# Optimization experiments

Hardware: AMD Instinct MI355X
Metric: run time of the kernel (lower is better)

## Reference

```python
import jax, jax.numpy as jnp
import numpy as np
import math

B, T, D = 2, 2048, 2048
N_HEADS, N_KV, HEAD_DIM = 16, 4, 128
INTER = 8192
MAX_POS = 4096
ROPE_BASE = 10000.0
EPS = 1e-6


def _rope_tables():
    inv_freq = 1.0 / (ROPE_BASE ** (jnp.arange(0, HEAD_DIM, 2, dtype=jnp.float32) / HEAD_DIM))
    t = jnp.arange(MAX_POS, dtype=jnp.float32)
    freqs = jnp.einsum('i,j->ij', t, inv_freq)          # [MAX_POS, HEAD_DIM//2]
    emb = jnp.concatenate([freqs, freqs], axis=-1)      # [MAX_POS, HEAD_DIM]
    return jnp.cos(emb), jnp.sin(emb)


def _apply_rope(x, cos, sin):
    # x: [B,H,T,Dh]; cos/sin: [B,T,Dh] (gathered by position_ids)
    c = cos[:, None, :, :]
    s = sin[:, None, :, :]
    x1 = x[..., ::2]
    x2 = x[..., 1::2]
    x_rot = jnp.stack([-x2, x1], axis=-1).reshape(x.shape)  # interleave(-x2, x1)
    return x * c + x_rot * s


def _rms_norm(x, w):
    var = jnp.mean(x * x, axis=-1, keepdims=True)
    return w * (x * jax.lax.rsqrt(var + EPS))


def setup_inputs() -> dict:
    key = jax.random.key(0)
    ks = jax.random.split(key, 10)
    s = 0.02
    hidden_states = jax.random.normal(ks[0], (B, T, D), dtype=jnp.float32)
    # additive causal mask
    causal = jnp.tril(jnp.ones((T, T), dtype=bool))
    attention_mask = jnp.where(causal, 0.0, -1e9).astype(jnp.float32)[None, None]
    position_ids = jnp.arange(B * T).reshape(B, T)  # values < MAX_POS
    return {
        'hidden_states': hidden_states,
        'attention_mask': attention_mask,
        'position_ids': position_ids,
        'attn_norm_w': jnp.ones((D,), jnp.float32),
        'mlp_norm_w': jnp.ones((D,), jnp.float32),
        'wq': jax.random.normal(ks[1], (D, N_HEADS * HEAD_DIM), jnp.float32) * s,
        'wk': jax.random.normal(ks[2], (D, N_KV * HEAD_DIM), jnp.float32) * s,
        'wv': jax.random.normal(ks[3], (D, N_KV * HEAD_DIM), jnp.float32) * s,
        'wo': jax.random.normal(ks[4], (N_HEADS * HEAD_DIM, D), jnp.float32) * s,
        'gate_w': jax.random.normal(ks[5], (D, D), jnp.float32) * s,
        'gate_b': jnp.zeros((D,), jnp.float32),
        'fc1_w': jax.random.normal(ks[6], (D, INTER), jnp.float32) * s,
        'fc2_w': jax.random.normal(ks[7], (INTER, D), jnp.float32) * s,
    }


def reference(hidden_states, attention_mask, position_ids, attn_norm_w, mlp_norm_w,
              wq, wk, wv, wo, gate_w, gate_b, fc1_w, fc2_w):
    b, t, _ = hidden_states.shape
    residual = hidden_states
    h = _rms_norm(hidden_states, attn_norm_w)

    # elementwise sigmoid output gate: [B,T,D] -> [B,H,T,Dh]
    gate = jax.nn.sigmoid(h @ gate_w + gate_b)
    gate = gate.reshape(b, t, N_HEADS, HEAD_DIM).transpose(0, 2, 1, 3)

    q = (h @ wq).reshape(b, t, N_HEADS, HEAD_DIM).transpose(0, 2, 1, 3)
    k = (h @ wk).reshape(b, t, N_KV, HEAD_DIM).transpose(0, 2, 1, 3)
    v = (h @ wv).reshape(b, t, N_KV, HEAD_DIM).transpose(0, 2, 1, 3)

    cos_t, sin_t = _rope_tables()
    cos = cos_t[position_ids]  # [B,T,Dh]
    sin = sin_t[position_ids]
    q = _apply_rope(q, cos, sin)
    k = _apply_rope(k, cos, sin)

    n_rep = N_HEADS // N_KV
    k = jnp.repeat(k, n_rep, axis=1)  # GQA expand to [B,H,T,Dh]
    v = jnp.repeat(v, n_rep, axis=1)

    scores = jnp.einsum('bhqd,bhkd->bhqk', q, k) / math.sqrt(HEAD_DIM)
    scores = scores + attention_mask
    attn = jax.nn.softmax(scores, axis=-1)
    out = jnp.einsum('bhqk,bhkd->bhqd', attn, v) * gate
    out = out.transpose(0, 2, 1, 3).reshape(b, t, N_HEADS * HEAD_DIM) @ wo

    h = residual + out
    residual = h
    h2 = _rms_norm(h, mlp_norm_w)
    mlp_out = jax.nn.silu(h2 @ fc1_w) @ fc2_w
    return residual + mlp_out
```

## Files before the change

### kernel.cpp

```cpp
#include <hip/hip_runtime.h>
#include <hip/hip_bf16.h>
#include <cstdint>
#include <cstddef>

#define BB 2
#define TT 2048
#define DD 2048
#define NH 16
#define NKV 4
#define HD 128
#define NI 8192
#define MM (BB*TT)

typedef __bf16 bf16x8 __attribute__((ext_vector_type(8)));
typedef float  f32x4  __attribute__((ext_vector_type(4)));

__device__ __forceinline__ void gload_lds16(const void* g, void* l) {
  __builtin_amdgcn_global_load_lds((__attribute__((address_space(1))) void*)g,
                                   (__attribute__((address_space(3))) void*)l,
                                   16, 0, 0);
}

__device__ __forceinline__ int xcd_swizzle(int wg, int nwg) {
  int xcd = wg & 7;
  int l = wg >> 3;
  int q = nwg >> 3, r = nwg & 7;
  return (xcd < r ? xcd * (q + 1) : r * (q + 1) + (xcd - r) * q) + l;
}

__global__ __launch_bounds__(128) void rope_tables_k(float* __restrict__ cosT,
                                                     float* __restrict__ sinT) {
  int pos = blockIdx.x;
  int d = threadIdx.x;
  int f = d & 63;
  float inv = powf(10000.0f, -((float)(2 * f)) / 128.0f);
  float ang = inv * (float)pos;
  cosT[pos * 128 + d] = cosf(ang);
  sinT[pos * 128 + d] = sinf(ang);
}

template <typename TIN>
__global__ __launch_bounds__(256) void transpose_to_bf16_k(const TIN* __restrict__ in,
                                                           __bf16* __restrict__ out,
                                                           int R, int C) {
  __shared__ float t[32][33];
  int c0 = blockIdx.x * 32, r0 = blockIdx.y * 32;
  int tx = threadIdx.x & 31;
  int ty = threadIdx.x >> 5;
#pragma unroll
  for (int i = 0; i < 4; i++) {
    int r = ty + i * 8;
    t[r][tx] = (float)in[(size_t)(r0 + r) * C + c0 + tx];
  }
  __syncthreads();
#pragma unroll
  for (int i = 0; i < 4; i++) {
    int r = ty + i * 8;
    out[(size_t)(c0 + r) * R + r0 + tx] = (__bf16)t[tx][r];
  }
}

__global__ __launch_bounds__(256) void rmsnorm_k(const float* __restrict__ x,
                                                 const float* __restrict__ w,
                                                 __bf16* __restrict__ out) {
  int row = blockIdx.x;
  const float* xr = x + (size_t)row * DD;
  int t = threadIdx.x;
  float4 a = ((const float4*)xr)[2 * t];
  float4 b = ((const float4*)xr)[2 * t + 1];
  float ss = a.x * a.x + a.y * a.y + a.z * a.z + a.w * a.w +
             b.x * b.x + b.y * b.y + b.z * b.z + b.w * b.w;
#pragma unroll
  for (int off = 32; off; off >>= 1) ss += __shfl_xor(ss, off, 64);
  __shared__ float red[4];
  if ((t & 63) == 0) red[t >> 6] = ss;
  __syncthreads();
  float tot = red[0] + red[1] + red[2] + red[3];
  float rs = rsqrtf(tot * (1.0f / DD) + 1e-6f);
  const float4 w1 = ((const float4*)w)[2 * t];
  const float4 w2 = ((const float4*)w)[2 * t + 1];
  bf16x8 ov;
  ov[0] = (__bf16)(a.x * rs * w1.x);
  ov[1] = (__bf16)(a.y * rs * w1.y);
  ov[2] = (__bf16)(a.z * rs * w1.z);
  ov[3] = (__bf16)(a.w * rs * w1.w);
  ov[4] = (__bf16)(b.x * rs * w2.x);
  ov[5] = (__bf16)(b.y * rs * w2.y);
  ov[6] = (__bf16)(b.z * rs * w2.z);
  ov[7] = (__bf16)(b.w * rs * w2.w);
  *(bf16x8*)(out + (size_t)row * DD + t * 8) = ov;
}

enum { G_QG = 0, G_RES = 1, G_SILU = 2, G_PART = 3 };

template <int EPI>
__global__ __launch_bounds__(512) void gemm256_k(
    const __bf16* __restrict__ A, const __bf16* __restrict__ Bt,
    __bf16* __restrict__ outB, float* __restrict__ outF,
    __bf16* __restrict__ outQ, __bf16* __restrict__ outG,
    const float* __restrict__ bias, const float* __restrict__ residual,
    const float* __restrict__ cosT, const float* __restrict__ sinT,
    const int* __restrict__ posids, int N, int K, int ldk, float oscale) {
  __shared__ __align__(16) __bf16 Ab[3][256 * 32];
  __shared__ __align__(16) __bf16 Bb[3][256 * 32];
  const int tid = threadIdx.x;
  const int lane = tid & 63;
  const int wid = tid >> 6;
  const int wr = wid >> 2;
  const int wc = wid & 3;
  const int fr = lane & 15;
  const int fg = lane >> 4;

  const int nwg = gridDim.x * gridDim.y;
  int wg = xcd_swizzle(blockIdx.y * gridDim.x + blockIdx.x, nwg);
  const int bx = wg % gridDim.x, by = wg / gridDim.x;
  const int m0 = by * 256;
  const int n0 = bx * 256;
  const int kz = blockIdx.z;
  const int kBase = kz * K;

  const int srow0 = wid * 32 + (lane >> 2);
  const int scol = (((lane & 3) ^ ((lane >> 3) & 3)) << 3);
  const __bf16* aS0 = A + (size_t)(m0 + srow0) * ldk + kBase + scol;
  const __bf16* aS1 = aS0 + (size_t)16 * ldk;
  const __bf16* bS0 = Bt + (size_t)(n0 + srow0) * ldk + kBase + scol;
  const __bf16* bS1 = bS0 + (size_t)16 * ldk;
  const int e0 = (wid * 2) * 512;
  const int e1 = (wid * 2 + 1) * 512;

  const int nt = K / 32;

#define STG_A0(kt, s) gload_lds16(aS0 + (kt) * 32, &Ab[(s)][e0]);
#define STG_A1(kt, s) gload_lds16(aS1 + (kt) * 32, &Ab[(s)][e1]);
#define STG_B0(kt, s) gload_lds16(bS0 + (kt) * 32, &Bb[(s)][e0]);
#define STG_B1(kt, s) gload_lds16(bS1 + (kt) * 32, &Bb[(s)][e1]);

  STG_A0(0, 0); STG_A1(0, 0); STG_B0(0, 0); STG_B1(0, 0);
  STG_A0(1, 1); STG_A1(1, 1); STG_B0(1, 1); STG_B1(1, 1);
  asm volatile("s_waitcnt vmcnt(4)" ::: "memory");
  __builtin_amdgcn_s_barrier();

  f32x4 acc[8][4];
#pragma unroll
  for (int i = 0; i < 8; i++)
#pragma unroll
    for (int j = 0; j < 4; j++) acc[i][j] = (f32x4){0.f, 0.f, 0.f, 0.f};

  const int asl = (fg ^ ((fr >> 1) & 3)) * 8;

  for (int t = 0; t < nt; ++t) {
    const int s = t % 3;
    const int sn = (t + 2) % 3;
    const bool dostage = (t + 2 < nt);
    bf16x8 bfr[4];

    {
      bf16x8 af[2];
#pragma unroll
      for (int mi = 0; mi < 2; mi++)
        af[mi] = *(const bf16x8*)&Ab[s][(wr * 128 + mi * 16 + fr) * 32 + asl];
#pragma unroll
      for (int ni = 0; ni < 4; ni++)
        bfr[ni] = *(const bf16x8*)&Bb[s][(wc * 64 + ni * 16 + fr) * 32 + asl];
      if (dostage) STG_A0(t + 2, sn);
      __builtin_amdgcn_s_barrier();
      asm volatile("s_waitcnt lgkmcnt(0)" ::: "memory");
      __builtin_amdgcn_sched_barrier(0);
      __builtin_amdgcn_s_setprio(1);
#pragma unroll
      for (int mi = 0; mi < 2; mi++)
#pragma unroll
        for (int ni = 0; ni < 4; ni++)
          acc[mi][ni] =
              __builtin_amdgcn_mfma_f32_16x16x32_bf16(af[mi], bfr[ni], acc[mi][ni], 0, 0, 0);
      __builtin_amdgcn_s_setprio(0);
      __builtin_amdgcn_s_barrier();
    }
#pragma unroll
    for (int ph = 1; ph < 4; ph++) {
      bf16x8 af[2];
#pragma unroll
      for (int mi = 0; mi < 2; mi++)
        af[mi] = *(const bf16x8*)&Ab[s][(wr * 128 + (ph * 2 + mi) * 16 + fr) * 32 + asl];
      if (dostage) {
        if (ph == 1) { STG_A1(t + 2, sn); }
        else if (ph == 2) { STG_B0(t + 2, sn); }
        else { STG_B1(t + 2, sn); }
      }
      __builtin_amdgcn_s_barrier();
      asm volatile("s_waitcnt lgkmcnt(0)" ::: "memory");
      __builtin_amdgcn_sched_barrier(0);
      __builtin_amdgcn_s_setprio(1);
#pragma unroll
      for (int mi = 0; mi < 2; mi++)
#pragma unroll
        for (int ni = 0; ni < 4; ni++)
          acc[ph * 2 + mi][ni] = __builtin_amdgcn_mfma_f32_16x16x32_bf16(
              af[mi], bfr[ni], acc[ph * 2 + mi][ni], 0, 0, 0);
      __builtin_amdgcn_s_setprio(0);
      if (ph == 3) {
        if (dostage) {
          asm volatile("s_waitcnt vmcnt(4)" ::: "memory");
        } else {
          asm volatile("s_waitcnt vmcnt(0)" ::: "memory");
        }
      }
      __builtin_amdgcn_s_barrier();
    }
  }
#undef STG_A0
#undef STG_A1
#undef STG_B0
#undef STG_B1

#pragma unroll
  for (int mi = 0; mi < 8; mi++) {
    const int row = m0 + wr * 128 + mi * 16 + fg * 4;
#pragma unroll
    for (int ni = 0; ni < 4; ni++) {
      const int col = n0 + wc * 64 + ni * 16 + fr;
#pragma unroll
      for (int j = 0; j < 4; j++) {
        float v = acc[mi][ni][j];
        const int r = row + j;
        if constexpr (EPI == G_QG) {
          float vp = __shfl_xor(v, 1, 64);
          if (n0 < 2048) {
            int pos = posids[r];
            int d = col & 127;
            float c = cosT[pos * 128 + d], sn2 = sinT[pos * 128 + d];
            float o = (col & 1) ? (v * c + vp * sn2) : (v * c - vp * sn2);
            outQ[(size_t)r * 2048 + col] = (__bf16)(o * oscale);
          } else {
            float xx = v + bias[col - 2048];
            outG[(size_t)r * 2048 + (col - 2048)] = (__bf16)(1.0f / (1.0f + expf(-xx)));
          }
        } else if constexpr (EPI == G_RES) {
          outF[(size_t)r * N + col] = v + residual[(size_t)r * N + col];
        } else if constexpr (EPI == G_SILU) {
          outB[(size_t)r * N + col] = (__bf16)(v / (1.0f + expf(-v)));
        } else {
          outB[(size_t)(kz * MM + r) * N + col] = (__bf16)v;
        }
      }
    }
  }
}

__global__ __launch_bounds__(256) void combine_k(const __bf16* __restrict__ parts,
                                                 const float* __restrict__ res,
                                                 float* __restrict__ out) {
  size_t i = ((size_t)blockIdx.x * 256 + threadIdx.x) * 8;
  bf16x8 p0 = *(const bf16x8*)&parts[i];
  bf16x8 p1 = *(const bf16x8*)&parts[(size_t)MM * 2048 + i];
  float4 a = *(const float4*)&res[i];
  float4 b = *(const float4*)&res[i + 4];
  float4 o0, o1;
  o0.x = (float)p0[0] + (float)p1[0] + a.x;
  o0.y = (float)p0[1] + (float)p1[1] + a.y;
  o0.z = (float)p0[2] + (float)p1[2] + a.z;
  o0.w = (float)p0[3] + (float)p1[3] + a.w;
  o1.x = (float)p0[4] + (float)p1[4] + b.x;
  o1.y = (float)p0[5] + (float)p1[5] + b.y;
  o1.z = (float)p0[6] + (float)p1[6] + b.z;
  o1.w = (float)p0[7] + (float)p1[7] + b.w;
  *(float4*)&out[i] = o0;
  *(float4*)&out[i + 4] = o1;
}

__global__ __launch_bounds__(256) void combine_rms_k(const __bf16* __restrict__ parts,
                                                     const float* __restrict__ res,
                                                     const float* __restrict__ w,
                                                     float* __restrict__ h1,
                                                     __bf16* __restrict__ h2) {
  const int row = blockIdx.x;
  const int t = threadIdx.x;
  const size_t i = (size_t)row * 2048 + t * 8;
  bf16x8 p0 = *(const bf16x8*)&parts[i];
  bf16x8 p1 = *(const bf16x8*)&parts[(size_t)MM * 2048 + i];
  float4 a = *(const float4*)&res[i];
  float4 b = *(const float4*)&res[i + 4];
  float v[8];
  v[0] = (float)p0[0] + (float)p1[0] + a.x;
  v[1] = (float)p0[1] + (float)p1[1] + a.y;
  v[2] = (float)p0[2] + (float)p1[2] + a.z;
  v[3] = (float)p0[3] + (float)p1[3] + a.w;
  v[4] = (float)p0[4] + (float)p1[4] + b.x;
  v[5] = (float)p0[5] + (float)p1[5] + b.y;
  v[6] = (float)p0[6] + (float)p1[6] + b.z;
  v[7] = (float)p0[7] + (float)p1[7] + b.w;
  float4 o0 = {v[0], v[1], v[2], v[3]};
  float4 o1 = {v[4], v[5], v[6], v[7]};
  *(float4*)&h1[i] = o0;
  *(float4*)&h1[i + 4] = o1;
  float ss = 0.f;
#pragma unroll
  for (int k = 0; k < 8; k++) ss += v[k] * v[k];
#pragma unroll
  for (int off = 32; off; off >>= 1) ss += __shfl_xor(ss, off, 64);
  __shared__ float red[4];
  if ((t & 63) == 0) red[t >> 6] = ss;
  __syncthreads();
  float tot = red[0] + red[1] + red[2] + red[3];
  float rs = rsqrtf(tot * (1.0f / DD) + 1e-6f);
  const float4 w1 = ((const float4*)w)[2 * t];
  const float4 w2 = ((const float4*)w)[2 * t + 1];
  bf16x8 ov;
  ov[0] = (__bf16)(v[0] * rs * w1.x);
  ov[1] = (__bf16)(v[1] * rs * w1.y);
  ov[2] = (__bf16)(v[2] * rs * w1.z);
  ov[3] = (__bf16)(v[3] * rs * w1.w);
  ov[4] = (__bf16)(v[4] * rs * w2.x);
  ov[5] = (__bf16)(v[5] * rs * w2.y);
  ov[6] = (__bf16)(v[6] * rs * w2.z);
  ov[7] = (__bf16)(v[7] * rs * w2.w);
  *(bf16x8*)(h2 + i) = ov;
}

__global__ __launch_bounds__(256) void gemm_kv_k(
    const __bf16* __restrict__ A, const __bf16* __restrict__ Bt,
    __bf16* __restrict__ kOut, __bf16* __restrict__ vOut,
    const float* __restrict__ cosT, const float* __restrict__ sinT,
    const int* __restrict__ posids, int K) {
  __shared__ __align__(16) __bf16 As[128 * 32];
  __shared__ __align__(16) __bf16 Bs[128 * 32];
  const int tid = threadIdx.x;
  const int lane = tid & 63;
  const int w = tid >> 6;
  const int wm = w >> 1, wn = w & 1;

  const int nwg = gridDim.x * gridDim.y;
  int wg = xcd_swizzle(blockIdx.y * gridDim.x + blockIdx.x, nwg);
  const int bx = wg % gridDim.x, by = wg / gridDim.x;
  const int m0 = by * 128;
  const int n0 = bx * 128;

  const int lr = lane >> 2;
  const int lc = (lane & 3) * 8;
  const __bf16* aSrc = A + (size_t)(m0 + 32 * w + lr) * K + lc;
  const __bf16* bSrc = Bt + (size_t)(n0 + 32 * w + lr) * K + lc;
  __bf16* aDst = &As[w * 1024];
  __bf16* bDst = &Bs[w * 1024];

  f32x4 acc[4][4];
#pragma unroll
  for (int i = 0; i < 4; i++)
#pragma unroll
    for (int j = 0; j < 4; j++) acc[i][j] = (f32x4){0.f, 0.f, 0.f, 0.f};

  const int fr = lane & 15;
  const int fc = (lane >> 4) * 8;

  for (int k0 = 0; k0 < K; k0 += 32) {
    __syncthreads();
    gload_lds16(aSrc + k0, aDst);
    gload_lds16(aSrc + k0 + (size_t)16 * K, aDst + 512);
    gload_lds16(bSrc + k0, bDst);
    gload_lds16(bSrc + k0 + (size_t)16 * K, bDst + 512);
    asm volatile("s_waitcnt vmcnt(0)" ::: "memory");
    __syncthreads();

    bf16x8 af[4], bfg[4];
#pragma unroll
    for (int i = 0; i < 4; i++)
      af[i] = *(const bf16x8*)&As[(wm * 64 + i * 16 + fr) * 32 + fc];
#pragma unroll
    for (int i = 0; i < 4; i++)
      bfg[i] = *(const bf16x8*)&Bs[(wn * 64 + i * 16 + fr) * 32 + fc];
#pragma unroll
    for (int mi = 0; mi < 4; mi++)
#pragma unroll
      for (int ni = 0; ni < 4; ni++)
        acc[mi][ni] =
            __builtin_amdgcn_mfma_f32_16x16x32_bf16(af[mi], bfg[ni], acc[mi][ni], 0, 0, 0);
  }

  const int fg = lane >> 4;
#pragma unroll
  for (int mi = 0; mi < 4; mi++) {
#pragma unroll
    for (int ni = 0; ni < 4; ni++) {
#pragma unroll
      for (int j = 0; j < 4; j++) {
        int row = m0 + wm * 64 + mi * 16 + fg * 4 + j;
        int col = n0 + wn * 64 + ni * 16 + fr;
        float v = acc[mi][ni][j];
        float vp = __shfl_xor(v, 1, 64);
        if (col < 512) {
          int pos = posids[row];
          int d = col & 127;
          float c = cosT[pos * 128 + d];
          float s = sinT[pos * 128 + d];
          float o = (col & 1) ? (v * c + vp * s) : (v * c - vp * s);
          kOut[(size_t)row * 512 + col] = (__bf16)o;
        } else {
          vOut[(size_t)row * 512 + (col - 512)] = (__bf16)v;
        }
      }
    }
  }
}

__global__ __launch_bounds__(256) void attn_k(const __bf16* __restrict__ Q,
                                              const __bf16* __restrict__ Kb,
                                              const __bf16* __restrict__ Vt,
                                              const __bf16* __restrict__ Gate,
                                              __bf16* __restrict__ Out) {
  __shared__ __align__(16) __bf16 Ks[2][64 * 128];
  __shared__ __align__(16) __bf16 Vs[2][128 * 64];
  __shared__ __align__(16) __bf16 Ps[4][16 * 64];
  const int tid = threadIdx.x;
  const int lane = tid & 63;
  const int w = tid >> 6;
  const int fr = lane & 15;
  const int fg = lane >> 4;

  const int nwg = gridDim.x * gridDim.y;
  int wg = xcd_swizzle(blockIdx.y * gridDim.x + blockIdx.x, nwg);
  const int qb = wg % gridDim.x;
  const int bh = wg / gridDim.x;
  const int q0 = qb * 64;
  const int b = bh >> 4, h = bh & 15;
  const int g = h >> 2;

  const size_t qrow = (size_t)(b * TT + q0 + w * 16 + fr);
  bf16x8 qf[4];
#pragma unroll
  for (int kt = 0; kt < 4; kt++)
    qf[kt] = *(const bf16x8*)&Q[qrow * 2048 + h * 128 + kt * 32 + fg * 8];

  const __bf16* kPtr[4];
  const __bf16* vPtr[4];
#pragma unroll
  for (int i = 0; i < 4; i++) {
    int krow = w * 16 + i * 4 + (lane >> 4);
    int kcol8 = (lane & 15) ^ (krow & 15);
    kPtr[i] = Kb + (size_t)(b * TT + krow) * 512 + g * 128 + kcol8 * 8;
    int dloc = w * 32 + i * 8 + (lane >> 3);
    int kv8 = (lane & 7) ^ (dloc & 7);
    vPtr[i] = Vt + (size_t)(g * 128 + dloc) * (size_t)MM + b * TT + kv8 * 8;
  }

  f32x4 o[8];
#pragma unroll
  for (int i = 0; i < 8; i++) o[i] = (f32x4){0.f, 0.f, 0.f, 0.f};
  float mrow[4] = {-3e38f, -3e38f, -3e38f, -3e38f};
  float lrow[4] = {0.f, 0.f, 0.f, 0.f};

  const int nsteps = qb + 1;

#pragma unroll
  for (int i = 0; i < 4; i++) {
    gload_lds16(kPtr[i], &Ks[0][w * 2048 + i * 512]);
    gload_lds16(vPtr[i], &Vs[0][w * 2048 + i * 512]);
  }
  __syncthreads();

  for (int t = 0; t < nsteps; t++) {
    const int cur = t & 1;
    const int kb = t * 64;
    if (t + 1 < nsteps) {
      const int nb = kb + 64;
#pragma unroll
      for (int i = 0; i < 4; i++) {
        gload_lds16(kPtr[i] + (size_t)nb * 512, &Ks[cur ^ 1][w * 2048 + i * 512]);
        gload_lds16(vPtr[i] + nb, &Vs[cur ^ 1][w * 2048 + i * 512]);
      }
    }

    f32x4 s[4];
#pragma unroll
    for (int nc = 0; nc < 4; nc++) s[nc] = (f32x4){0.f, 0.f, 0.f, 0.f};
#pragma unroll
    for (int nc = 0; nc < 4; nc++)
#pragma unroll
      for (int kt = 0; kt < 4; kt++) {
        bf16x8 kf = *(const bf16x8*)&Ks[cur][(nc * 16 + fr) * 128 + (((kt * 4 + fg) ^ fr) << 3)];
        s[nc] = __builtin_amdgcn_mfma_f32_16x16x32_bf16(qf[kt], kf, s[nc], 0, 0, 0);
      }

    float alpha[4];
#pragma unroll
    for (int j = 0; j < 4; j++) {
      const int qr = q0 + w * 16 + fg * 4 + j;
      float pv[4];
#pragma unroll
      for (int nc = 0; nc < 4; nc++) {
        int kc = kb + nc * 16 + fr;
        float val = s[nc][j];
        if (kc > qr) val = -1e9f;
        pv[nc] = val;
      }
      float tmx = fmaxf(fmaxf(pv[0], pv[1]), fmaxf(pv[2], pv[3]));
      tmx = fmaxf(tmx, __shfl_xor(tmx, 1, 64));
      tmx = fmaxf(tmx, __shfl_xor(tmx, 2, 64));
      tmx = fmaxf(tmx, __shfl_xor(tmx, 4, 64));
      tmx = fmaxf(tmx, __shfl_xor(tmx, 8, 64));
      float mnew = fmaxf(mrow[j], tmx);
      alpha[j] = __expf(mrow[j] - mnew);
      mrow[j] = mnew;
      float rsum = 0.f;
      const int q = fg * 4 + j;
#pragma unroll
      for (int nc = 0; nc < 4; nc++) {
        float e = __expf(pv[nc] - mnew);
        rsum += e;
        Ps[w][q * 64 + (((nc * 2 + (fr >> 3)) ^ (q & 7)) << 3) + (fr & 7)] = (__bf16)e;
      }
      rsum += __shfl_xor(rsum, 1, 64);
      rsum += __shfl_xor(rsum, 2, 64);
      rsum += __shfl_xor(rsum, 4, 64);
      rsum += __shfl_xor(rsum, 8, 64);
      lrow[j] = lrow[j] * alpha[j] + rsum;
    }
#pragma unroll
    for (int nd = 0; nd < 8; nd++)
#pragma unroll
      for (int j = 0; j < 4; j++) o[nd][j] *= alpha[j];

    bf16x8 pa[2];
#pragma unroll
    for (int sl = 0; sl < 2; sl++)
      pa[sl] = *(const bf16x8*)&Ps[w][fr * 64 + (((sl * 4 + fg) ^ (fr & 7)) << 3)];
#pragma unroll
    for (int nd = 0; nd < 8; nd++)
#pragma unroll
      for (int sl = 0; sl < 2; sl++) {
        bf16x8 vf =
            *(const bf16x8*)&Vs[cur][(nd * 16 + fr) * 64 + (((sl * 4 + fg) ^ (fr & 7)) << 3)];
        o[nd] = __builtin_amdgcn_mfma_f32_16x16x32_bf16(pa[sl], vf, o[nd], 0, 0, 0);
      }
    __syncthreads();
  }

  float invl[4];
#pragma unroll
  for (int j = 0; j < 4; j++) invl[j] = 1.0f / lrow[j];
#pragma unroll
  for (int nd = 0; nd < 8; nd++) {
#pragma unroll
    for (int j = 0; j < 4; j++) {
      int row = q0 + w * 16 + fg * 4 + j;
      int d = nd * 16 + fr;
      size_t idx = (size_t)(b * TT + row) * 2048 + h * 128 + d;
      float val = o[nd][j] * invl[j] * (float)Gate[idx];
      Out[idx] = (__bf16)val;
    }
  }
}

extern "C" void kernel_launch(void* const* d_in, const int* in_sizes, int n_in,
                              void* d_out, int out_size, void* d_ws, size_t ws_size,
                              hipStream_t stream) {
  const float* hidden = (const float*)d_in[0];
  const int* posids = (const int*)d_in[2];
  const float* attn_w = (const float*)d_in[3];
  const float* mlp_w = (const float*)d_in[4];
  const float* wq = (const float*)d_in[5];
  const float* wk = (const float*)d_in[6];
  const float* wv = (const float*)d_in[7];
  const float* wo = (const float*)d_in[8];
  const float* gw = (const float*)d_in[9];
  const float* gb = (const float*)d_in[10];
  const float* f1 = (const float*)d_in[11];
  const float* f2 = (const float*)d_in[12];

  char* p = (char*)d_ws;
  auto alloc = [&](size_t n) {
    char* r = p;
    p += (n + 255) & ~(size_t)255;
    return r;
  };
  __bf16* wqg_t = (__bf16*)alloc((size_t)4096 * 2048 * 2);
  __bf16* wkv_t = (__bf16*)alloc((size_t)1024 * 2048 * 2);
  __bf16* wo_t = (__bf16*)alloc((size_t)2048 * 2048 * 2);
  __bf16* f1_t = (__bf16*)alloc((size_t)NI * 2048 * 2);
  __bf16* f2_t = (__bf16*)alloc((size_t)2048 * NI * 2);
  __bf16* h_bf = (__bf16*)alloc((size_t)MM * DD * 2);
  float* h1 = (float*)alloc((size_t)MM * 2048 * 4);

  char* regionA = alloc((size_t)64 * 1024 * 1024);
  __bf16* q_bf = (__bf16*)(regionA);
  __bf16* gate_bf = (__bf16*)(regionA + (size_t)16 * 1024 * 1024);
  __bf16* attn_g = (__bf16*)(regionA + (size_t)32 * 1024 * 1024);
  __bf16* k_bf = (__bf16*)(regionA + (size_t)48 * 1024 * 1024);
  __bf16* v_bf = (__bf16*)(regionA + (size_t)52 * 1024 * 1024);
  __bf16* v_t = (__bf16*)(regionA + (size_t)56 * 1024 * 1024);
  float* cosT = (float*)(regionA + (size_t)60 * 1024 * 1024);
  float* sinT = (float*)(regionA + (size_t)62 * 1024 * 1024);
  __bf16* mlp1 = (__bf16*)(regionA);
  __bf16* parts_wo = (__bf16*)(regionA);
  __bf16* parts_fc2 = (__bf16*)f1_t;

  rope_tables_k<<<4096, 128, 0, stream>>>(cosT, sinT);

  transpose_to_bf16_k<float><<<dim3(64, 64), 256, 0, stream>>>(wq, wqg_t, 2048, 2048);
  transpose_to_bf16_k<float><<<dim3(64, 64), 256, 0, stream>>>(gw, wqg_t + (size_t)2048 * 2048, 2048, 2048);
  transpose_to_bf16_k<float><<<dim3(16, 64), 256, 0, stream>>>(wk, wkv_t, 2048, 512);
  transpose_to_bf16_k<float><<<dim3(16, 64), 256, 0, stream>>>(wv, wkv_t + (size_t)512 * 2048, 2048, 512);
  transpose_to_bf16_k<float><<<dim3(64, 64), 256, 0, stream>>>(wo, wo_t, 2048, 2048);
  transpose_to_bf16_k<float><<<dim3(256, 64), 256, 0, stream>>>(f1, f1_t, 2048, NI);
  transpose_to_bf16_k<float><<<dim3(64, 256), 256, 0, stream>>>(f2, f2_t, NI, 2048);

  rmsnorm_k<<<MM, 256, 0, stream>>>(hidden, attn_w, h_bf);

  const float qsc = 0.08838834764831845f;
  gemm256_k<G_QG><<<dim3(16, 16), 512, 0, stream>>>(
      h_bf, wqg_t, nullptr, nullptr, q_bf, gate_bf, gb, nullptr, cosT, sinT, posids,
      4096, 2048, 2048, qsc);
  gemm_kv_k<<<dim3(8, 32), 256, 0, stream>>>(h_bf, wkv_t, k_bf, v_bf, cosT, sinT, posids, 2048);

  transpose_to_bf16_k<__bf16><<<dim3(16, 128), 256, 0, stream>>>(v_bf, v_t, MM, 512);

  attn_k<<<dim3(32, 32), 256, 0, stream>>>(q_bf, k_bf, v_t, gate_bf, attn_g);

  gemm256_k<G_PART><<<dim3(8, 16, 2), 512, 0, stream>>>(
      attn_g, wo_t, parts_wo, nullptr, nullptr, nullptr, nullptr, nullptr, nullptr, nullptr,
      nullptr, 2048, 1024, 2048, 1.0f);
  combine_rms_k<<<MM, 256, 0, stream>>>(parts_wo, hidden, mlp_w, h1, h_bf);

  gemm256_k<G_SILU><<<dim3(32, 16), 512, 0, stream>>>(
      h_bf, f1_t, mlp1, nullptr, nullptr, nullptr, nullptr, nullptr, nullptr, nullptr, nullptr,
      NI, 2048, 2048, 1.0f);

  gemm256_k<G_PART><<<dim3(8, 16, 2), 512, 0, stream>>>(
      mlp1, f2_t, parts_fc2, nullptr, nullptr, nullptr, nullptr, nullptr, nullptr, nullptr,
      nullptr, 2048, 4096, NI, 1.0f);

  combine_k<<<4096, 256, 0, stream>>>(parts_fc2, h1, (float*)d_out);
}
```

Before: 880.2 us.

## Restructure GEMM mainloop to BK=64 double buffer with quadrant-phased MFMA schedule

The 256x256 GEMM main loop moves from a triple-buffered K-step of 32 to a double-buffered K-step of 64, with a new XOR swizzle on 64-wide LDS rows. Each tile is split into four A/B quadrant phases, and the next tiles' loads are staged into the current buffer while the last quadrants are still being consumed. This halves the number of loop iterations and barriers per unit of K and gives each phase more MFMAs to hide LDS reads. In exchange it holds more fragment registers at once and relies on intricate buffer-reuse ordering that could race if the waitcnt or barrier placement is wrong.

```diff
diff --git a/kernel.cpp b/kernel.cpp
--- a/kernel.cpp
+++ b/kernel.cpp
@@ -101,8 +101,8 @@
     const float* __restrict__ bias, const float* __restrict__ residual,
     const float* __restrict__ cosT, const float* __restrict__ sinT,
     const int* __restrict__ posids, int N, int K, int ldk, float oscale) {
-  __shared__ __align__(16) __bf16 Ab[3][256 * 32];
-  __shared__ __align__(16) __bf16 Bb[3][256 * 32];
+  __shared__ __align__(16) __bf16 Ab[2][256 * 64];
+  __shared__ __align__(16) __bf16 Bb[2][256 * 64];
   const int tid = threadIdx.x;
   const int lane = tid & 63;
   const int wid = tid >> 6;
@@ -119,99 +119,111 @@
   const int kz = blockIdx.z;
   const int kBase = kz * K;
 
-  const int srow0 = wid * 32 + (lane >> 2);
-  const int scol = (((lane & 3) ^ ((lane >> 3) & 3)) << 3);
-  const __bf16* aS0 = A + (size_t)(m0 + srow0) * ldk + kBase + scol;
-  const __bf16* aS1 = aS0 + (size_t)16 * ldk;
-  const __bf16* bS0 = Bt + (size_t)(n0 + srow0) * ldk + kBase + scol;
-  const __bf16* bS1 = bS0 + (size_t)16 * ldk;
-  const int e0 = (wid * 2) * 512;
-  const int e1 = (wid * 2 + 1) * 512;
-
-  const int nt = K / 32;
-
-#define STG_A0(kt, s) gload_lds16(aS0 + (kt) * 32, &Ab[(s)][e0]);
-#define STG_A1(kt, s) gload_lds16(aS1 + (kt) * 32, &Ab[(s)][e1]);
-#define STG_B0(kt, s) gload_lds16(bS0 + (kt) * 32, &Bb[(s)][e0]);
-#define STG_B1(kt, s) gload_lds16(bS1 + (kt) * 32, &Bb[(s)][e1]);
-
-  STG_A0(0, 0); STG_A1(0, 0); STG_B0(0, 0); STG_B1(0, 0);
-  STG_A0(1, 1); STG_A1(1, 1); STG_B0(1, 1); STG_B1(1, 1);
-  asm volatile("s_waitcnt vmcnt(4)" ::: "memory");
+  const int rofs = lane >> 3;
+  const int swz = ((lane & 7) ^ rofs) * 8;
+  const int gA0 = ((wid & 4) << 5) + ((wid & 3) << 4);
+  const int gB0 = ((wid >> 1) << 6) + ((wid & 1) << 4);
+  const __bf16* aSrcB = A + (size_t)(m0 + rofs) * ldk + kBase + swz;
+  const __bf16* bSrcB = Bt + (size_t)(n0 + rofs) * ldk + kBase + swz;
+
+  const int nt = K / 64;
+
+#define STGA(buf, h, T)                                                              \
+  {                                                                                  \
+    const int g0_ = gA0 + (h) * 64;                                                  \
+    gload_lds16(aSrcB + (size_t)g0_ * ldk + (size_t)(T) * 64, &Ab[buf][g0_ * 64]);   \
+    gload_lds16(aSrcB + (size_t)(g0_ + 8) * ldk + (size_t)(T) * 64,                  \
+                &Ab[buf][(g0_ + 8) * 64]);                                           \
+  }
+#define STGB(buf, h, T)                                                              \
+  {                                                                                  \
+    const int g0_ = gB0 + (h) * 32;                                                  \
+    gload_lds16(bSrcB + (size_t)g0_ * ldk + (size_t)(T) * 64, &Bb[buf][g0_ * 64]);   \
+    gload_lds16(bSrcB + (size_t)(g0_ + 8) * ldk + (size_t)(T) * 64,                  \
+                &Bb[buf][(g0_ + 8) * 64]);                                           \
+  }
+#define RD_A(dst, buf, mh)                                                             \
+  _Pragma("unroll") for (int mt = 0; mt < 4; mt++)                                     \
+  _Pragma("unroll") for (int kk = 0; kk < 2; kk++)                                     \
+      dst[mt][kk] = *(const bf16x8*)&Ab[buf][(wr * 128 + (mh) * 64 + mt * 16 + fr) * 64 + \
+                                             (((kk * 4 + fg) ^ (fr & 7)) << 3)];
+#define RD_B(dst, buf, nh)                                                             \
+  _Pragma("unroll") for (int nt2 = 0; nt2 < 2; nt2++)                                  \
+  _Pragma("unroll") for (int kk = 0; kk < 2; kk++)                                     \
+      dst[nt2][kk] = *(const bf16x8*)&Bb[buf][(wc * 64 + (nh) * 32 + nt2 * 16 + fr) * 64 + \
+                                              (((kk * 4 + fg) ^ (fr & 7)) << 3)];
+#define MFMA16(a, b, MH, NH)                                                           \
+  _Pragma("unroll") for (int mt = 0; mt < 4; mt++)                                     \
+  _Pragma("unroll") for (int nt2 = 0; nt2 < 2; nt2++)                                  \
+  _Pragma("unroll") for (int kk = 0; kk < 2; kk++)                                     \
+      acc[(MH) * 4 + mt][(NH) * 2 + nt2] = __builtin_amdgcn_mfma_f32_16x16x32_bf16(    \
+          a[mt][kk], b[nt2][kk], acc[(MH) * 4 + mt][(NH) * 2 + nt2], 0, 0, 0);
+#define PHASE_SYNC                                        \
+  __builtin_amdgcn_s_barrier();                           \
+  asm volatile("s_waitcnt lgkmcnt(0)" ::: "memory");      \
+  __builtin_amdgcn_sched_barrier(0);                      \
+  __builtin_amdgcn_s_setprio(1);
+#define PHASE_END                                         \
+  __builtin_amdgcn_s_setprio(0);                          \
   __builtin_amdgcn_s_barrier();
 
+#define TILE(T, CUR, OTH, S0, S123, VMSTR)                \
+  {                                                       \
+    bf16x8 a0[4][2], a1[4][2], b0[2][2], b1[2][2];        \
+    RD_A(a0, CUR, 0);                                     \
+    RD_B(b0, CUR, 0);                                     \
+    if (S0) STGB(OTH, 0, (T) + 1);                        \
+    PHASE_SYNC;                                           \
+    MFMA16(a0, b0, 0, 0);                                 \
+    PHASE_END;                                            \
+    RD_B(b1, CUR, 1);                                     \
+    if (S123) STGA(CUR, 0, (T) + 2);                      \
+    PHASE_SYNC;                                           \
+    MFMA16(a0, b1, 0, 1);                                 \
+    PHASE_END;                                            \
+    RD_A(a1, CUR, 1);                                     \
+    if (S123) STGB(CUR, 1, (T) + 2);                      \
+    PHASE_SYNC;                                           \
+    MFMA16(a1, b1, 1, 1);                                 \
+    PHASE_END;                                            \
+    if (S123) STGA(CUR, 1, (T) + 2);                      \
+    __builtin_amdgcn_s_barrier();                         \
+    __builtin_amdgcn_sched_barrier(0);                    \
+    __builtin_amdgcn_s_setprio(1);                        \
+    MFMA16(a1, b0, 1, 0);                                 \
+    __builtin_amdgcn_s_setprio(0);                        \
+    asm volatile("s_waitcnt " VMSTR ::: "memory");        \
+    __builtin_amdgcn_s_barrier();                         \
+  }
+
   f32x4 acc[8][4];
 #pragma unroll
   for (int i = 0; i < 8; i++)
 #pragma unroll
     for (int j = 0; j < 4; j++) acc[i][j] = (f32x4){0.f, 0.f, 0.f, 0.f};
 
-  const int asl = (fg ^ ((fr >> 1) & 3)) * 8;
-
-  for (int t = 0; t < nt; ++t) {
-    const int s = t % 3;
-    const int sn = (t + 2) % 3;
-    const bool dostage = (t + 2 < nt);
-    bf16x8 bfr[4];
-
-    {
-      bf16x8 af[2];
-#pragma unroll
-      for (int mi = 0; mi < 2; mi++)
-        af[mi] = *(const bf16x8*)&Ab[s][(wr * 128 + mi * 16 + fr) * 32 + asl];
-#pragma unroll
-      for (int ni = 0; ni < 4; ni++)
-        bfr[ni] = *(const bf16x8*)&Bb[s][(wc * 64 + ni * 16 + fr) * 32 + asl];
-      if (dostage) STG_A0(t + 2, sn);
-      __builtin_amdgcn_s_barrier();
-      asm volatile("s_waitcnt lgkmcnt(0)" ::: "memory");
-      __builtin_amdgcn_sched_barrier(0);
-      __builtin_amdgcn_s_setprio(1);
-#pragma unroll
-      for (int mi = 0; mi < 2; mi++)
-#pragma unroll
-        for (int ni = 0; ni < 4; ni++)
-          acc[mi][ni] =
-              __builtin_amdgcn_mfma_f32_16x16x32_bf16(af[mi], bfr[ni], acc[mi][ni], 0, 0, 0);
-      __builtin_amdgcn_s_setprio(0);
-      __builtin_amdgcn_s_barrier();
+  STGB(0, 0, 0); STGA(0, 0, 0); STGB(0, 1, 0); STGA(0, 1, 0);
+  STGA(1, 0, 1); STGB(1, 1, 1); STGA(1, 1, 1);
+  asm volatile("s_waitcnt vmcnt(6)" ::: "memory");
+  __builtin_amdgcn_s_barrier();
+
+  for (int t = 0; t < nt; t += 2) {
+    if (t + 2 < nt) {
+      TILE(t, 0, 1, true, true, "vmcnt(6)");
+      TILE(t + 1, 1, 0, true, true, "vmcnt(6)");
+    } else {
+      TILE(t, 0, 1, true, false, "vmcnt(0)");
+      TILE(t + 1, 1, 0, false, false, "vmcnt(0)");
     }
-#pragma unroll
-    for (int ph = 1; ph < 4; ph++) {
-      bf16x8 af[2];
-#pragma unroll
-      for (int mi = 0; mi < 2; mi++)
-        af[mi] = *(const bf16x8*)&Ab[s][(wr * 128 + (ph * 2 + mi) * 16 + fr) * 32 + asl];
-      if (dostage) {
-        if (ph == 1) { STG_A1(t + 2, sn); }
-        else if (ph == 2) { STG_B0(t + 2, sn); }
-        else { STG_B1(t + 2, sn); }
-      }
-      __builtin_amdgcn_s_barrier();
-      asm volatile("s_waitcnt lgkmcnt(0)" ::: "memory");
-      __builtin_amdgcn_sched_barrier(0);
-      __builtin_amdgcn_s_setprio(1);
-#pragma unroll
-      for (int mi = 0; mi < 2; mi++)
-#pragma unroll
-        for (int ni = 0; ni < 4; ni++)
-          acc[ph * 2 + mi][ni] = __builtin_amdgcn_mfma_f32_16x16x32_bf16(
-              af[mi], bfr[ni], acc[ph * 2 + mi][ni], 0, 0, 0);
-      __builtin_amdgcn_s_setprio(0);
-      if (ph == 3) {
-        if (dostage) {
-          asm volatile("s_waitcnt vmcnt(4)" ::: "memory");
-        } else {
-          asm volatile("s_waitcnt vmcnt(0)" ::: "memory");
-        }
-      }
-      __builtin_amdgcn_s_barrier();
-    }
-  }
-#undef STG_A0
-#undef STG_A1
-#undef STG_B0
-#undef STG_B1
+  }
+#undef TILE
+#undef PHASE_SYNC
+#undef PHASE_END
+#undef MFMA16
+#undef RD_A
+#undef RD_B
+#undef STGA
+#undef STGB
 
 #pragma unroll
   for (int mi = 0; mi < 8; mi++) {
```

Result: slower. 2.559 ms (+190.7%).
